# Performance work log

Hardware: AMD Instinct MI355X
Metric: run time of the kernel (lower is better)

The kernel has to match this reference:

```python
import jax, jax.numpy as jnp
import numpy as np


def leaky(x):
    return jnp.where(x > 0, x, 0.2 * x)


def conv(x, w, b, s, p):
    y = jax.lax.conv_general_dilated(x, w, (s, s), [(p, p), (p, p)],
                                     dimension_numbers=('NCHW', 'OIHW', 'NCHW'))
    return y + b[None, :, None, None]


def maxpool2s1(x):
    return jax.lax.reduce_window(x, -jnp.inf, jax.lax.max, (1, 1, 2, 2), (1, 1, 1, 1), 'VALID')


def bn_eval(x, g, b, m, v):
    scale = g / jnp.sqrt(v + 1e-5)
    return (x - m[None, :, None, None]) * scale[None, :, None, None] + b[None, :, None, None]


def adaptive_avg_pool(x, oh, ow):
    # matches torch AdaptiveAvgPool2d window rule: [floor(i*H/o), ceil((i+1)*H/o))
    B, C, H, W = x.shape
    rows = []
    for i in range(oh):
        hs, he = (i * H) // oh, -((-(i + 1) * H) // oh)
        cols = []
        for j in range(ow):
            ws, we = (j * W) // ow, -((-(j + 1) * W) // ow)
            cols.append(x[:, :, hs:he, ws:we].mean((2, 3)))
        rows.append(jnp.stack(cols, -1))
    return jnp.stack(rows, -2)  # [B,C,oh,ow]


def forward(x, tw1, tb1, tw2, tb2, tw3, tb3, tw4, tb4,
            sw1, sb1, bn1_g, bn1_b, bn1_m, bn1_v,
            sw2, sb2, bn2_g, bn2_b, bn2_m, bn2_v,
            cw, cb, ew1, eb1, ew2, eb2, ew3, eb3):
    B = x.shape[0]
    E, K = ew1.shape[0], 2
    # --- scout router (BN in eval mode with running stats) ---
    h = jax.nn.relu(bn_eval(conv(x, sw1, sb1, 4, 3), bn1_g, bn1_b, bn1_m, bn1_v))
    h = jax.nn.relu(bn_eval(conv(h, sw2, sb2, 2, 1), bn2_g, bn2_b, bn2_m, bn2_v))
    logits = h.mean((2, 3)) @ cw.T + cb                       # [B,E]
    gate = jax.nn.softmax(logits, axis=-1)
    topk_p, topk_i = jax.lax.top_k(gate, K)                   # [B,K]
    topk_p = topk_p / (topk_p.sum(-1, keepdims=True) + 1e-6)
    # --- shared trunk ---
    t = maxpool2s1(leaky(conv(x, tw1, tb1, 4, 1)))            # 224->56->55
    t = maxpool2s1(leaky(conv(t, tw2, tb2, 2, 2)))            # 55->28->27
    t = leaky(conv(t, tw3, tb3, 1, 1))                        # 27
    t = maxpool2s1(leaky(conv(t, tw4, tb4, 1, 1)))            # 27->26
    t = adaptive_avg_pool(t, 3, 3)                            # [B,128,3,3]
    flat = t.reshape(B, -1)                                   # [B,1152]
    # --- MoE head: dense per-expert MLP, masked weighted combine ---
    h1 = leaky(jnp.einsum('bi,eoi->beo', flat, ew1) + eb1[None])   # [B,E,1024]
    h2 = leaky(jnp.einsum('beh,eoh->beo', h1, ew2) + eb2[None])    # [B,E,512]
    h3 = jnp.einsum('beh,eoh->beo', h2, ew3) + eb3[None]           # [B,E,feat]
    onehot = (topk_i[:, :, None] == jnp.arange(E)[None, None, :])  # [B,K,E]
    comb_w = jnp.sum(topk_p[:, :, None] * onehot, axis=1)          # [B,E]
    out = jnp.einsum('beo,be->bo', h3, comb_w)                     # [B,feat]
    return out


def setup_inputs() -> dict:
    key = jax.random.key(0)
    ks = jax.random.split(key, 32)
    W = 0.02
    d = {}
    d['x'] = jax.random.normal(ks[0], (256, 3, 224, 224), jnp.float32)
    d['tw1'] = jax.random.normal(ks[1], (16, 3, 3, 3), jnp.float32) * W
    d['tb1'] = jnp.zeros((16,), jnp.float32)
    d['tw2'] = jax.random.normal(ks[2], (32, 16, 5, 5), jnp.float32) * W
    d['tb2'] = jnp.zeros((32,), jnp.float32)
    d['tw3'] = jax.random.normal(ks[3], (64, 32, 3, 3), jnp.float32) * W
    d['tb3'] = jnp.zeros((64,), jnp.float32)
    d['tw4'] = jax.random.normal(ks[4], (128, 64, 3, 3), jnp.float32) * W
    d['tb4'] = jnp.zeros((128,), jnp.float32)
    d['sw1'] = jax.random.normal(ks[5], (16, 3, 7, 7), jnp.float32) * W
    d['sb1'] = jnp.zeros((16,), jnp.float32)
    d['bn1_g'] = jnp.ones((16,), jnp.float32)
    d['bn1_b'] = jnp.zeros((16,), jnp.float32)
    d['bn1_m'] = jnp.zeros((16,), jnp.float32)
    d['bn1_v'] = jnp.ones((16,), jnp.float32)
    d['sw2'] = jax.random.normal(ks[6], (32, 16, 3, 3), jnp.float32) * W
    d['sb2'] = jnp.zeros((32,), jnp.float32)
    d['bn2_g'] = jnp.ones((32,), jnp.float32)
    d['bn2_b'] = jnp.zeros((32,), jnp.float32)
    d['bn2_m'] = jnp.zeros((32,), jnp.float32)
    d['bn2_v'] = jnp.ones((32,), jnp.float32)
    d['cw'] = jax.random.normal(ks[7], (3, 32), jnp.float32) * W
    d['cb'] = jnp.zeros((3,), jnp.float32)
    d['ew1'] = jax.random.normal(ks[8], (3, 1024, 1152), jnp.float32) * W
    d['eb1'] = jnp.zeros((3, 1024), jnp.float32)
    d['ew2'] = jax.random.normal(ks[9], (3, 512, 1024), jnp.float32) * W
    d['eb2'] = jnp.zeros((3, 512), jnp.float32)
    d['ew3'] = jax.random.normal(ks[10], (3, 512, 512), jnp.float32) * W
    d['eb3'] = jnp.zeros((3, 512), jnp.float32)
    return d


def reference(x, tw1, tb1, tw2, tb2, tw3, tb3, tw4, tb4,
              sw1, sb1, bn1_g, bn1_b, bn1_m, bn1_v,
              sw2, sb2, bn2_g, bn2_b, bn2_m, bn2_v,
              cw, cb, ew1, eb1, ew2, eb2, ew3, eb3):
    return forward(x, tw1, tb1, tw2, tb2, tw3, tb3, tw4, tb4,
                   sw1, sb1, bn1_g, bn1_b, bn1_m, bn1_v,
                   sw2, sb2, bn2_g, bn2_b, bn2_m, bn2_v,
                   cw, cb, ew1, eb1, ew2, eb2, ew3, eb3)
```

## Files before the change

kernel.cpp:

```cpp
#include <hip/hip_runtime.h>

#define DEV static __device__ __forceinline__

constexpr int BATCH = 256;

DEV float leakyf(float x){ return x > 0.f ? x : 0.2f * x; }

typedef _Float16 f16x8 __attribute__((ext_vector_type(8)));
typedef float f32x4 __attribute__((ext_vector_type(4)));

DEV f16x8 max8(f16x8 a, f16x8 b){
  f16x8 r;
  #pragma unroll
  for (int j = 0; j < 8; ++j) r[j] = a[j] > b[j] ? a[j] : b[j];
  return r;
}

template<int IC,int OC>
DEV void wpackM_body(int i, const float* __restrict__ w, _Float16* __restrict__ wp){
  constexpr int F = OC/16;
  int j = i & 7, L = (i >> 3) & 63, rest = i >> 9;
  int f = rest % F; int q2 = rest / F; int s = q2 % (IC/32); int t = q2 / (IC/32);
  int oc = f*16 + (L & 15), ic = s*32 + (L >> 4)*8 + j;
  wp[i] = (_Float16)w[((size_t)oc*IC + ic)*9 + t];
}

template<int OC,int K>
DEV void wpackS_body(int i, const float* __restrict__ w, _Float16* __restrict__ wp){
  constexpr int F = OC/16, KWP = (K+1)/2;
  int j = i & 7, L = (i >> 3) & 63, rest = i >> 9;
  int f = rest % F, s = rest / F;
  int kh = s / KWP, kwp = s % KWP;
  int k = (L >> 4)*8 + j;
  int kw = 2*kwp + (k >> 4), ic = k & 15;
  int oc = f*16 + (L & 15);
  float v = (kw < K) ? w[((size_t)(oc*16 + ic)*K + kh)*K + kw] : 0.f;
  wp[i] = (_Float16)v;
}

DEV void wpackF_body(int i, const float* __restrict__ sw1,
                     const float* __restrict__ tw1, _Float16* __restrict__ wp){
  int j = i & 7, L = (i >> 3) & 63, rest = i >> 9;
  int nf = rest & 1, s = rest >> 1;
  int k = s*32 + (L >> 4)*8 + j;
  int oc = L & 15;
  int t = k / 48, c = k % 48;
  int dr = (t >> 1) - 1, dc = (t & 1) - 1;
  int ic = c >> 4, pr = (c >> 2) & 3, pc = c & 3;
  float v = 0.f;
  if (nf == 0){
    int kh = 4*dr + pr + 3, kw = 4*dc + pc + 3;
    if (kh >= 0 && kh < 7 && kw >= 0 && kw < 7) v = sw1[((oc*3 + ic)*7 + kh)*7 + kw];
  } else {
    int kh = 4*dr + pr + 1, kw = 4*dc + pc + 1;
    if (kh >= 0 && kh < 3 && kw >= 0 && kw < 3) v = tw1[((oc*3 + ic)*3 + kh)*3 + kw];
  }
  wp[i] = (_Float16)v;
}

__global__ __launch_bounds__(256) void wpackAll_k(
    const float* __restrict__ tw3, _Float16* __restrict__ wpk3,
    const float* __restrict__ tw4, _Float16* __restrict__ wpk4,
    const float* __restrict__ tw2, _Float16* __restrict__ wp2,
    const float* __restrict__ sw2, _Float16* __restrict__ wps2,
    const float* __restrict__ sw1, const float* __restrict__ tw1,
    _Float16* __restrict__ wpf){
  const int b = blockIdx.x;
  if (b < 72){
    wpackM_body<32,64>(b*256 + threadIdx.x, tw3, wpk3);
  } else if (b < 360){
    wpackM_body<64,128>((b-72)*256 + threadIdx.x, tw4, wpk4);
  } else if (b < 420){
    wpackS_body<32,5>((b-360)*256 + threadIdx.x, tw2, wp2);
  } else if (b < 444){
    wpackS_body<32,3>((b-420)*256 + threadIdx.x, sw2, wps2);
  } else {
    wpackF_body((b-444)*256 + threadIdx.x, sw1, tw1, wpf);
  }
}

template<int KTOT>
__global__ __launch_bounds__(256) void wpackGh_k(const float* __restrict__ w, int N,
    _Float16* __restrict__ wp){
  const int NF = N >> 4, KT = KTOT >> 5;
  const int total = NF * KT * 512;
  const int e = blockIdx.y;
  w  += (size_t)e * N * KTOT;
  wp += (size_t)e * total;
  int i = blockIdx.x*256 + threadIdx.x;
  if (i >= total) return;
  int j = i & 7, L = (i >> 3) & 63, rest = i >> 9;
  int nf = rest % NF, t = rest / NF;
  int n = nf*16 + (L & 15), k = t*32 + (L >> 4)*8 + j;
  wp[i] = (_Float16)w[(size_t)n*KTOT + k];
}

__global__ __launch_bounds__(256) void fusedM_k(
    const float* __restrict__ x,
    const _Float16* __restrict__ W,
    const float* __restrict__ sb, const float* __restrict__ cb_,
    const float* __restrict__ g, const float* __restrict__ bt,
    const float* __restrict__ mn, const float* __restrict__ vr,
    _Float16* __restrict__ s1out, _Float16* __restrict__ c1out){
  __shared__ __align__(16) _Float16 Ah[3*58*64];
  const int tid = threadIdx.x;
  const int n = blockIdx.x / 28, oh0 = (blockIdx.x % 28) * 2;

  if (tid < 48){
    int rr = tid >> 4, side = (tid >> 3) & 1, q = tid & 7;
    int col = side ? 57 : 0;
    *(int4*)((char*)Ah + (((rr*58 + col) << 7) + q*16)) = (int4){0,0,0,0};
  }

  {
    const int m = tid & 63;
    const bool mok = (m < 56);
    const int cc = m + 1;
    int rc0 = tid >> 6;
    int ic   = (rc0 == 3) ? 0 : rc0;
    int ridx = (rc0 == 3) ? 1 : 0;
    #pragma unroll
    for (int j = 0; j < 9; ++j){
      const int ih = 4*oh0 - 4 + ridx;
      if (mok){
        float4 v = {0.f,0.f,0.f,0.f};
        if (ih >= 0)
          v = *(const float4*)(x + ((size_t)(n*3 + ic)*224 + ih)*224 + 4*m);
        const int rr = ridx >> 2, pr = ridx & 3;
        int boff = (((rr*58 + cc) << 7) + ic*32 + pr*8) ^ ((cc & 7) << 4);
        _Float16 h4[4] = {(_Float16)v.x, (_Float16)v.y, (_Float16)v.z, (_Float16)v.w};
        *(unsigned long long*)((char*)Ah + boff) = *(unsigned long long*)h4;
      }
      ic += 1; ridx += 1;
      if (ic >= 3){ ic -= 3; ridx += 1; }
    }
  }
  __syncthreads();

  const int wid = tid >> 6, lane = tid & 63;
  const int kg8 = (lane >> 4) * 8;
  f32x4 acc[2][2];
  #pragma unroll
  for (int mi = 0; mi < 2; ++mi)
    #pragma unroll
    for (int nf = 0; nf < 2; ++nf) acc[mi][nf] = (f32x4){0.f,0.f,0.f,0.f};

  #pragma unroll
  for (int s = 0; s < 6; ++s){
    const int kk = s*32 + kg8;
    const int t = kk / 48, c0 = kk - t*48;
    const int ra = t >> 1, ca = t & 1;
    f16x8 ah[2];
    #pragma unroll
    for (int mi = 0; mi < 2; ++mi){
      const int m = 2*wid + mi;
      const int rowsel = m >> 2;
      const int ow = (m & 3)*16 + (lane & 15);
      const int owc = ow > 55 ? 55 : ow;
      const int col = owc + ca;
      const int bidx = ((((rowsel + ra)*58 + col) << 7) + c0*2) ^ ((col & 7) << 4);
      ah[mi] = *(const f16x8*)((const char*)Ah + bidx);
    }
    #pragma unroll
    for (int nf = 0; nf < 2; ++nf){
      const f16x8 bw = *(const f16x8*)(W + (s*2 + nf)*512 + lane*8);
      #pragma unroll
      for (int mi = 0; mi < 2; ++mi)
        acc[mi][nf] = __builtin_amdgcn_mfma_f32_16x16x32_f16(ah[mi], bw, acc[mi][nf], 0,0,0);
    }
  }

  const int oc = lane & 15;
  const float sbv = sb[oc];
  const float scv = g[oc] * __frsqrt_rn(vr[oc] + 1e-5f);
  const float mnv = mn[oc], btv = bt[oc], cbv = cb_[oc];
  #pragma unroll
  for (int mi = 0; mi < 2; ++mi){
    const int m = 2*wid + mi;
    const int row = oh0 + (m >> 2);
    const int owb = (m & 3)*16 + (lane >> 4)*4;
    #pragma unroll
    for (int r = 0; r < 4; ++r){
      const int ow = owb + r;
      if (ow >= 56) continue;
      float vs = acc[mi][0][r] + sbv;
      vs = fmaxf((vs - mnv)*scv + btv, 0.f);
      const size_t o = (((size_t)n*56 + row)*56 + ow)*16 + oc;
      s1out[o] = (_Float16)vs;
      c1out[o] = (_Float16)leakyf(acc[mi][1][r] + cbv);
    }
  }
}

template<int OC,int K,int P,int IH,int IW,int ACT,bool OUT16,bool GATE,bool POOLIN>
__global__ __launch_bounds__(256) void convS_k(
    const _Float16* __restrict__ in,
    const _Float16* __restrict__ W,
    const float* __restrict__ bias,
    const float* __restrict__ bng, const float* __restrict__ bnb,
    const float* __restrict__ bnm, const float* __restrict__ bnv,
    float* __restrict__ outF, _Float16* __restrict__ outH,
    float* __restrict__ gsum){
  constexpr int F = OC/16, KWP = (K+1)/2;
  constexpr int RW = POOLIN ? (IW+1) : IW;
  __shared__ __align__(16) _Float16 A[K*60*16];
  __shared__ float gred[32];

  const int tid = threadIdx.x;
  const int n = blockIdx.x / 28, oh = blockIdx.x % 28;

  if (GATE && tid < 32) gred[tid] = 0.f;

  for (int i = tid; i < K*60*2; i += 256){
    int half = i & 1; int p = i >> 1;
    int c = p % 60; int r = p / 60;
    int ih = 2*oh - P + r, iw = c - P;
    int4 v = {0,0,0,0};
    if (ih >= 0 && ih < IH && iw >= 0 && iw < IW){
      const _Float16* q = in + (((size_t)n*(POOLIN ? IH+1 : IH) + ih)*RW + iw)*16 + half*8;
      if (POOLIN){
        f16x8 a = *(const f16x8*)q;
        f16x8 b = *(const f16x8*)(q + 16);
        f16x8 cc = *(const f16x8*)(q + RW*16);
        f16x8 d = *(const f16x8*)(q + RW*16 + 16);
        f16x8 mx = max8(max8(a, b), max8(cc, d));
        v = *(int4*)&mx;
      } else {
        v = *(const int4*)q;
      }
    }
    int byte = ((r*60 + c)*32 + half*16) ^ (((c>>1)&7) << 4);
    *(int4*)((char*)A + byte) = v;
  }
  __syncthreads();

  const int wid = tid >> 6, lane = tid & 63;
  const int fsel = wid & 1, mb = wid >> 1;
  const int ow_l = min(mb*16 + (lane & 15), 27);
  const int ic0b = ((lane >> 4) & 1) * 16;
  const int kwo  = (lane >> 4) >> 1;

  f32x4 acc = {0.f,0.f,0.f,0.f};
  #pragma unroll
  for (int kh = 0; kh < K; ++kh){
    #pragma unroll
    for (int kwp = 0; kwp < KWP; ++kwp){
      const int kw = 2*kwp + kwo;
      const int c = 2*ow_l + kw;
      int byte = ((kh*60 + c)*32 + ic0b) ^ (((c>>1)&7) << 4);
      f16x8 a = *(const f16x8*)((const char*)A + byte);
      const int s = kh*KWP + kwp;
      const f16x8 b = *(const f16x8*)(W + (s*F + fsel)*512 + lane*8);
      acc = __builtin_amdgcn_mfma_f32_16x16x32_f16(a, b, acc, 0,0,0);
    }
  }

  const int oc = fsel*16 + (lane & 15);
  float bv = bias[oc], sc = 1.f, mm = 0.f, bb = 0.f;
  if (ACT == 1){
    sc = bng[oc] * __frsqrt_rn(bnv[oc] + 1e-5f);
    mm = bnm[oc]; bb = bnb[oc];
  }
  float lsum = 0.f;
  #pragma unroll
  for (int r = 0; r < 4; ++r){
    const int ow = mb*16 + (lane >> 4)*4 + r;
    if (ow >= 28) continue;
    float v = acc[r] + bv;
    if (ACT == 1) v = fmaxf((v - mm)*sc + bb, 0.f);
    else          v = leakyf(v);
    if (GATE){
      lsum += v;
    } else {
      const size_t o = (((size_t)n*28 + oh)*28 + ow)*OC + oc;
      if (OUT16) outH[o] = (_Float16)v;
      else       outF[o] = v;
    }
  }
  if (GATE){
    atomicAdd(&gred[oc], lsum);
    __syncthreads();
    if (tid < 32) atomicAdd(&gsum[n*32 + tid], gred[tid]);
  }
}

template<int IC,int OC,bool POOLIN>
__global__ __launch_bounds__(256) void convM_k(
    const _Float16* __restrict__ Ag,
    const _Float16* __restrict__ W,
    const float* __restrict__ bias,
    _Float16* __restrict__ Out)
{
  constexpr int S = IC/32, FTOT = OC/16, FW = FTOT/2;
  constexpr int ICB = IC*2, ICG = ICB/16;
  __shared__ __align__(16) char A[4*34*ICB];

  const int tid = threadIdx.x;
  const int bx = blockIdx.x;
  const int n = bx / 14, pr = bx % 14;
  const int oh0 = pr * 2;

  for (int g = tid; g < 4*34*ICG; g += 256){
    int r = g / (34*ICG);
    int rem = g - r*(34*ICG);
    int c = rem / ICG, q = rem - c*ICG;
    int ir = oh0 + r - 1, icol = c - 1;
    int4 v = {0,0,0,0};
    if (ir >= 0 && ir < 27 && icol >= 0 && icol < 27){
      if (POOLIN){
        const _Float16* p0 = Ag + (((size_t)n*28 + ir)*28 + icol)*IC + q*8;
        f16x8 a = *(const f16x8*)p0;
        f16x8 b = *(const f16x8*)(p0 + IC);
        f16x8 cc = *(const f16x8*)(p0 + 28*IC);
        f16x8 d = *(const f16x8*)(p0 + 28*IC + IC);
        f16x8 mx = max8(max8(a, b), max8(cc, d));
        v = *(int4*)&mx;
      } else {
        v = *(const int4*)(Ag + (((size_t)n*27 + ir)*27 + icol)*IC + q*8);
      }
    }
    int off = (r*34 + c)*ICB + q*16;
    int swz = off ^ ((c & 7) << 4);
    *(int4*)(A + swz) = v;
  }
  __syncthreads();

  const int wid = tid >> 6, lane = tid & 63;
  const int rsel = wid & 1, ocq = wid >> 1;
  const int c0 = lane & 15, kg = (lane >> 4) * 16;
  const int colb0 = c0*ICB + kg, colb1 = (16 + c0)*ICB + kg;
  int msk[3];
  #pragma unroll
  for (int kw = 0; kw < 3; ++kw) msk[kw] = ((c0 + kw) & 7) << 4;

  f32x4 acc[2][FW];
  #pragma unroll
  for (int m = 0; m < 2; ++m)
    #pragma unroll
    for (int f = 0; f < FW; ++f) acc[m][f] = (f32x4){0.f,0.f,0.f,0.f};

  #pragma unroll
  for (int kh = 0; kh < 3; ++kh){
    #pragma unroll
    for (int kw = 0; kw < 3; ++kw){
      #pragma unroll
      for (int s = 0; s < S; ++s){
        const int fr0 = (((kh*3 + kw)*S + s)*FTOT + ocq*FW) * 512 + lane*8;
        f16x8 b[FW];
        #pragma unroll
        for (int f = 0; f < FW; ++f)
          b[f] = *(const f16x8*)(W + fr0 + f*512);
        const int base = ((rsel + kh)*34 + kw)*ICB + s*64;
        const int o0 = (base + colb0) ^ msk[kw];
        const int o1 = (base + colb1) ^ msk[kw];
        f16x8 a0 = *(const f16x8*)(A + o0);
        f16x8 a1 = *(const f16x8*)(A + o1);
        #pragma unroll
        for (int f = 0; f < FW; ++f){
          acc[0][f] = __builtin_amdgcn_mfma_f32_16x16x32_f16(a0, b[f], acc[0][f], 0,0,0);
          acc[1][f] = __builtin_amdgcn_mfma_f32_16x16x32_f16(a1, b[f], acc[1][f], 0,0,0);
        }
      }
    }
  }

  const int orow = oh0 + rsel;
  if (orow >= 27) return;
  #pragma unroll
  for (int f = 0; f < FW; ++f){
    const int oc = (ocq*FW + f)*16 + c0;
    const float bv = bias[oc];
    #pragma unroll
    for (int m = 0; m < 2; ++m){
      #pragma unroll
      for (int r = 0; r < 4; ++r){
        const int ow = m*16 + (lane >> 4)*4 + r;
        if (ow >= 27) continue;
        float v = leakyf(acc[m][f][r] + bv);
        Out[(((size_t)n*27 + orow)*27 + ow)*OC + oc] = (_Float16)v;
      }
    }
  }
}

template<int KTOT,int ACT>
__global__ __launch_bounds__(256) void gemmH_k(
    const _Float16* __restrict__ A, long strideA,
    const _Float16* __restrict__ W,
    const float* __restrict__ bias, int N,
    _Float16* __restrict__ OutH){
  const int e = blockIdx.z;
  A += (size_t)e * strideA;
  const int NF = N >> 4, KT = KTOT >> 5;
  W += (size_t)e * NF * KT * 512;
  const float* bs = bias + (size_t)e * N;
  const size_t ob = (size_t)e * 256 * N;

  const int tid = threadIdx.x, wid = tid >> 6, lane = tid & 63;
  const int mblk = blockIdx.x * 32;
  const int nf = blockIdx.y * 4 + wid;
  const int r0 = mblk + (lane & 15);
  const int kof = (lane >> 4) * 8;

  f32x4 acc0 = {0,0,0,0}, acc1 = {0,0,0,0};
  for (int t = 0; t < KT; ++t){
    const int k = t*32 + kof;
    f16x8 a0 = *(const f16x8*)(A + (size_t)r0*KTOT + k);
    f16x8 a1 = *(const f16x8*)(A + (size_t)(r0+16)*KTOT + k);
    const f16x8 b = *(const f16x8*)(W + ((size_t)t*NF + nf)*512 + lane*8);
    acc0 = __builtin_amdgcn_mfma_f32_16x16x32_f16(a0, b, acc0, 0,0,0);
    acc1 = __builtin_amdgcn_mfma_f32_16x16x32_f16(a1, b, acc1, 0,0,0);
  }
  const int n = nf*16 + (lane & 15);
  const float bv = bs[n];
  #pragma unroll
  for (int mi = 0; mi < 2; ++mi){
    f32x4 a = mi ? acc1 : acc0;
    #pragma unroll
    for (int r = 0; r < 4; ++r){
      const int m = mblk + mi*16 + (lane >> 4)*4 + r;
      float v = a[r] + bv;
      if (ACT == 1) v = leakyf(v);
      OutH[ob + (size_t)m*N + n] = (_Float16)v;
    }
  }
}

__global__ __launch_bounds__(256) void gemmC_k(
    const _Float16* __restrict__ A,
    const _Float16* __restrict__ W,
    const float* __restrict__ b3,
    const float* __restrict__ combw,
    float* __restrict__ out){
  const int tid = threadIdx.x, wid = tid >> 6, lane = tid & 63;
  const int mblk = blockIdx.x * 16;
  const int nf = blockIdx.y * 4 + wid;
  const int r0 = mblk + (lane & 15);
  const int kof = (lane >> 4) * 8;
  const int n = nf*16 + (lane & 15);

  f32x4 oacc = {0.f,0.f,0.f,0.f};
  #pragma unroll
  for (int e = 0; e < 3; ++e){
    const _Float16* Ae = A + (size_t)e * 256 * 512;
    const _Float16* We = W + (size_t)e * 32 * 16 * 512;
    f32x4 acc = {0.f,0.f,0.f,0.f};
    for (int t = 0; t < 16; ++t){
      f16x8 a = *(const f16x8*)(Ae + (size_t)r0*512 + t*32 + kof);
      const f16x8 b = *(const f16x8*)(We + ((size_t)t*32 + nf)*512 + lane*8);
      acc = __builtin_amdgcn_mfma_f32_16x16x32_f16(a, b, acc, 0,0,0);
    }
    const float bv = b3[e*512 + n];
    #pragma unroll
    for (int r = 0; r < 4; ++r){
      const int m = mblk + (lane >> 4)*4 + r;
      oacc[r] += combw[m*3 + e] * (acc[r] + bv);
    }
  }
  #pragma unroll
  for (int r = 0; r < 4; ++r){
    const int m = mblk + (lane >> 4)*4 + r;
    out[(size_t)m*512 + n] = oacc[r];
  }
}

__global__ __launch_bounds__(256) void gate2_k(const float* __restrict__ gsum,
                                               const float* __restrict__ cw,
                                               const float* __restrict__ cb,
                                               float* __restrict__ comb){
  int n = blockIdx.x * 256 + threadIdx.x;
  if (n >= BATCH) return;
  float mch[32];
  #pragma unroll
  for (int c = 0; c < 32; ++c) mch[c] = gsum[n*32 + c] / 784.f;
  float lg[3];
  #pragma unroll
  for (int e = 0; e < 3; ++e){
    float a = cb[e];
    #pragma unroll
    for (int c = 0; c < 32; ++c) a += mch[c] * cw[e*32 + c];
    lg[e] = a;
  }
  float m = fmaxf(lg[0], fmaxf(lg[1], lg[2]));
  float ex[3], sum = 0.f;
  #pragma unroll
  for (int e = 0; e < 3; ++e){ ex[e] = expf(lg[e] - m); sum += ex[e]; }
  float pr[3];
  #pragma unroll
  for (int e = 0; e < 3; ++e) pr[e] = ex[e] / sum;
  int i1 = 0;
  if (pr[1] > pr[0]) i1 = 1;
  if (pr[2] > pr[i1]) i1 = 2;
  int i2 = -1;
  for (int e = 0; e < 3; ++e){
    if (e == i1) continue;
    if (i2 < 0 || pr[e] > pr[i2]) i2 = e;
  }
  float s12 = pr[i1] + pr[i2] + 1e-6f;
  float cmb[3] = {0.f, 0.f, 0.f};
  cmb[i1] = pr[i1] / s12;
  cmb[i2] = pr[i2] / s12;
  comb[n*3 + 0] = cmb[0];
  comb[n*3 + 1] = cmb[1];
  comb[n*3 + 2] = cmb[2];
}

__global__ __launch_bounds__(256) void papool2_k(const _Float16* __restrict__ in,
                                                 _Float16* __restrict__ flat16){
  __shared__ float red[2][128][9];
  const int n = blockIdx.x;
  const int tid = threadIdx.x;
  const int h = tid >> 7, c = tid & 127;
  const _Float16* p = in + (size_t)n * 729 * 128 + c;

  float sum[9];
  #pragma unroll
  for (int j = 0; j < 9; ++j) sum[j] = 0.f;

  float prev[27], cur[27];
  const int r0 = h * 13;
  #pragma unroll
  for (int rr = 0; rr < 14; ++rr){
    const int r = r0 + rr;
    #pragma unroll
    for (int cc = 0; cc < 27; ++cc)
      cur[cc] = (float)p[(size_t)(r*27 + cc) * 128];
    if (rr > 0){
      const int pr = r - 1;
      const bool b0 = (pr < 9), b1 = (pr >= 8) && (pr < 18), b2 = (pr >= 17);
      #pragma unroll
      for (int cc = 0; cc < 26; ++cc){
        float v = fmaxf(fmaxf(prev[cc], prev[cc+1]), fmaxf(cur[cc], cur[cc+1]));
        if (b0){
          if (cc < 9)             sum[0] += v;
          if (cc >= 8 && cc < 18) sum[1] += v;
          if (cc >= 17)           sum[2] += v;
        }
        if (b1){
          if (cc < 9)             sum[3] += v;
          if (cc >= 8 && cc < 18) sum[4] += v;
          if (cc >= 17)           sum[5] += v;
        }
        if (b2){
          if (cc < 9)             sum[6] += v;
          if (cc >= 8 && cc < 18) sum[7] += v;
          if (cc >= 17)           sum[8] += v;
        }
      }
    }
    #pragma unroll
    for (int cc = 0; cc < 27; ++cc) prev[cc] = cur[cc];
  }

  #pragma unroll
  for (int j = 0; j < 9; ++j) red[h][c][j] = sum[j];
  __syncthreads();

  if (tid < 128){
    const float rcp[9] = {1.f/81, 1.f/90, 1.f/81, 1.f/90, 1.f/100, 1.f/90,
                          1.f/81, 1.f/90, 1.f/81};
    _Float16* o = flat16 + (size_t)n * 1152 + tid * 9;
    #pragma unroll
    for (int j = 0; j < 9; ++j)
      o[j] = (_Float16)((red[0][tid][j] + red[1][tid][j]) * rcp[j]);
  }
}

extern "C" void kernel_launch(void* const* d_in, const int* in_sizes, int n_in,
                              void* d_out, int out_size, void* d_ws, size_t ws_size,
                              hipStream_t stream){
  const float* x    = (const float*)d_in[0];
  const float* tw1  = (const float*)d_in[1];  const float* tb1 = (const float*)d_in[2];
  const float* tw2  = (const float*)d_in[3];  const float* tb2 = (const float*)d_in[4];
  const float* tw3  = (const float*)d_in[5];  const float* tb3 = (const float*)d_in[6];
  const float* tw4  = (const float*)d_in[7];  const float* tb4 = (const float*)d_in[8];
  const float* sw1  = (const float*)d_in[9];  const float* sb1 = (const float*)d_in[10];
  const float* bn1g = (const float*)d_in[11]; const float* bn1b = (const float*)d_in[12];
  const float* bn1m = (const float*)d_in[13]; const float* bn1v = (const float*)d_in[14];
  const float* sw2  = (const float*)d_in[15]; const float* sb2 = (const float*)d_in[16];
  const float* bn2g = (const float*)d_in[17]; const float* bn2b = (const float*)d_in[18];
  const float* bn2m = (const float*)d_in[19]; const float* bn2v = (const float*)d_in[20];
  const float* cw   = (const float*)d_in[21]; const float* cb  = (const float*)d_in[22];
  const float* ew1  = (const float*)d_in[23]; const float* eb1 = (const float*)d_in[24];
  const float* ew2  = (const float*)d_in[25]; const float* eb2 = (const float*)d_in[26];
  const float* ew3  = (const float*)d_in[27]; const float* eb3 = (const float*)d_in[28];
  float* out = (float*)d_out;

  float* ws = (float*)d_ws;
  size_t off = 0;
  float* comb   = ws + off; off += 768;
  _Float16* flat16 = (_Float16*)(ws + off); off += 147456;
  float* gsum   = ws + off; off += BATCH * 32;
  _Float16* wpk3 = (_Float16*)(ws + off); off += 9216;
  _Float16* wpk4 = (_Float16*)(ws + off); off += 36864;
  _Float16* wp2  = (_Float16*)(ws + off); off += 7680;
  _Float16* wps2 = (_Float16*)(ws + off); off += 3072;
  _Float16* wpf  = (_Float16*)(ws + off); off += 3072;
  off += 16;
  float* bufA   = ws + off; off += 13778944;
  off += 16;
  float* bufB   = ws + off; off += 23887872;
  off += 16;
  (void)ws_size; (void)in_sizes; (void)n_in; (void)out_size;

  _Float16* s1h = (_Float16*)bufA;
  _Float16* c1h = (_Float16*)bufB;
  _Float16* c2h = (_Float16*)(bufB + 14000000);
  _Float16* C3u = (_Float16*)bufA;
  _Float16* c4h = (_Float16*)bufB;

  _Float16* hb = (_Float16*)bufB;
  size_t uo = 0;
  _Float16* ewp1 = hb + uo; uo += 3538944;
  _Float16* ewp2 = hb + uo; uo += 1572864;
  _Float16* ewp3 = hb + uo; uo += 786432;
  _Float16* h1   = hb + uo; uo += 786432;
  _Float16* h2   = hb + uo; uo += 393216;

  dim3 blk(256);

  hipMemsetAsync(gsum, 0, BATCH * 32 * sizeof(float), stream);
  wpackAll_k<<<dim3(468), blk, 0, stream>>>(
      tw3, wpk3, tw4, wpk4, tw2, wp2, sw2, wps2, sw1, tw1, wpf);

  fusedM_k<<<dim3(BATCH*28), blk, 0, stream>>>(
      x, wpf, sb1, tb1, bn1g, bn1b, bn1m, bn1v, s1h, c1h);

  convS_k<32,3,1,56,56,1,false,true,false><<<dim3(BATCH*28), blk, 0, stream>>>(
      s1h, wps2, sb2, bn2g, bn2b, bn2m, bn2v, nullptr, nullptr, gsum);
  gate2_k<<<dim3(1), blk, 0, stream>>>(gsum, cw, cb, comb);

  convS_k<32,5,2,55,55,0,true,false,true><<<dim3(BATCH*28), blk, 0, stream>>>(
      c1h, wp2, tb2, nullptr, nullptr, nullptr, nullptr, nullptr, c2h, nullptr);

  convM_k<32,64,true><<<dim3(BATCH*14), blk, 0, stream>>>(
      c2h, wpk3, tb3, C3u);

  convM_k<64,128,false><<<dim3(BATCH*14), blk, 0, stream>>>(
      C3u, wpk4, tb4, c4h);

  papool2_k<<<dim3(BATCH), blk, 0, stream>>>(c4h, flat16);

  wpackGh_k<1152><<<dim3(4608,3), blk, 0, stream>>>(ew1, 1024, ewp1);
  wpackGh_k<1024><<<dim3(2048,3), blk, 0, stream>>>(ew2,  512, ewp2);
  wpackGh_k< 512><<<dim3(1024,3), blk, 0, stream>>>(ew3,  512, ewp3);

  gemmH_k<1152,1><<<dim3(8,16,3), blk, 0, stream>>>(
      flat16, 0L, ewp1, eb1, 1024, h1);
  gemmH_k<1024,1><<<dim3(8,8,3), blk, 0, stream>>>(
      h1, 256L*1024, ewp2, eb2, 512, h2);
  gemmC_k<<<dim3(16,8), blk, 0, stream>>>(
      h2, ewp3, eb3, comb, out);
}
```

Baseline: 265.9 us.

## Merge kernel launches: fold expert weight packing, both small convs, and gating

Folds the three expert-weight packing kernels into the initial weight-pack kernel, merges the two independent small convolutions into one launch split by block index, and moves the gate softmax/top-k computation into the final combine GEMM. Buffers are reassigned so the packed expert weights live in bufA beyond the activations that use it. The aim is fewer kernel launches and serialization gaps, and letting independent work share the GPU. The merged conv kernel uses the larger shared-memory footprint for both halves, which may reduce occupancy, and gate logic is recomputed per block of the final GEMM.

Result: faster. 257.1 us (-3.3%).

```diff
diff --git a/kernel.cpp b/kernel.cpp
--- a/kernel.cpp
+++ b/kernel.cpp
@@ -58,41 +58,53 @@
   wp[i] = (_Float16)v;
 }
 
-__global__ __launch_bounds__(256) void wpackAll_k(
+template<int KTOT>
+DEV void wpackG_body(int i, int e, const float* __restrict__ w, int N,
+                     _Float16* __restrict__ wp){
+  const int NF = N >> 4;
+  const int total = NF * (KTOT >> 5) * 512;
+  w  += (size_t)e * N * KTOT;
+  wp += (size_t)e * total;
+  int j = i & 7, L = (i >> 3) & 63, rest = i >> 9;
+  int nf = rest % NF, t = rest / NF;
+  int n = nf*16 + (L & 15), k = t*32 + (L >> 4)*8 + j;
+  wp[i] = (_Float16)w[(size_t)n*KTOT + k];
+}
+
+__global__ __launch_bounds__(256) void wpackX_k(
     const float* __restrict__ tw3, _Float16* __restrict__ wpk3,
     const float* __restrict__ tw4, _Float16* __restrict__ wpk4,
     const float* __restrict__ tw2, _Float16* __restrict__ wp2,
     const float* __restrict__ sw2, _Float16* __restrict__ wps2,
     const float* __restrict__ sw1, const float* __restrict__ tw1,
-    _Float16* __restrict__ wpf){
+    _Float16* __restrict__ wpf,
+    const float* __restrict__ ew1, _Float16* __restrict__ ewp1,
+    const float* __restrict__ ew2, _Float16* __restrict__ ewp2,
+    const float* __restrict__ ew3, _Float16* __restrict__ ewp3){
   const int b = blockIdx.x;
+  const int tid = threadIdx.x;
   if (b < 72){
-    wpackM_body<32,64>(b*256 + threadIdx.x, tw3, wpk3);
+    wpackM_body<32,64>(b*256 + tid, tw3, wpk3);
   } else if (b < 360){
-    wpackM_body<64,128>((b-72)*256 + threadIdx.x, tw4, wpk4);
+    wpackM_body<64,128>((b-72)*256 + tid, tw4, wpk4);
   } else if (b < 420){
-    wpackS_body<32,5>((b-360)*256 + threadIdx.x, tw2, wp2);
+    wpackS_body<32,5>((b-360)*256 + tid, tw2, wp2);
   } else if (b < 444){
-    wpackS_body<32,3>((b-420)*256 + threadIdx.x, sw2, wps2);
+    wpackS_body<32,3>((b-420)*256 + tid, sw2, wps2);
+  } else if (b < 468){
+    wpackF_body((b-444)*256 + tid, sw1, tw1, wpf);
   } else {
-    wpackF_body((b-444)*256 + threadIdx.x, sw1, tw1, wpf);
-  }
-}
-
-template<int KTOT>
-__global__ __launch_bounds__(256) void wpackGh_k(const float* __restrict__ w, int N,
-    _Float16* __restrict__ wp){
-  const int NF = N >> 4, KT = KTOT >> 5;
-  const int total = NF * KT * 512;
-  const int e = blockIdx.y;
-  w  += (size_t)e * N * KTOT;
-  wp += (size_t)e * total;
-  int i = blockIdx.x*256 + threadIdx.x;
-  if (i >= total) return;
-  int j = i & 7, L = (i >> 3) & 63, rest = i >> 9;
-  int nf = rest % NF, t = rest / NF;
-  int n = nf*16 + (L & 15), k = t*32 + (L >> 4)*8 + j;
-  wp[i] = (_Float16)w[(size_t)n*KTOT + k];
+    int t = b - 468;
+    if (t < 13824){
+      wpackG_body<1152>((t % 4608)*256 + tid, t / 4608, ew1, 1024, ewp1);
+    } else if (t < 19968){
+      int t2 = t - 13824;
+      wpackG_body<1024>((t2 % 2048)*256 + tid, t2 / 2048, ew2, 512, ewp2);
+    } else {
+      int t3 = t - 19968;
+      wpackG_body<512>((t3 % 1024)*256 + tid, t3 / 1024, ew3, 512, ewp3);
+    }
+  }
 }
 
 __global__ __launch_bounds__(256) void fusedM_k(
@@ -193,7 +205,7 @@
 }
 
 template<int OC,int K,int P,int IH,int IW,int ACT,bool OUT16,bool GATE,bool POOLIN>
-__global__ __launch_bounds__(256) void convS_k(
+DEV void convS_body(int bx, int tid, _Float16* A, float* gred,
     const _Float16* __restrict__ in,
     const _Float16* __restrict__ W,
     const float* __restrict__ bias,
@@ -203,11 +215,8 @@
     float* __restrict__ gsum){
   constexpr int F = OC/16, KWP = (K+1)/2;
   constexpr int RW = POOLIN ? (IW+1) : IW;
-  __shared__ __align__(16) _Float16 A[K*60*16];
-  __shared__ float gred[32];
-
-  const int tid = threadIdx.x;
-  const int n = blockIdx.x / 28, oh = blockIdx.x % 28;
+
+  const int n = bx / 28, oh = bx % 28;
 
   if (GATE && tid < 32) gred[tid] = 0.f;
 
@@ -281,6 +290,26 @@
     atomicAdd(&gred[oc], lsum);
     __syncthreads();
     if (tid < 32) atomicAdd(&gsum[n*32 + tid], gred[tid]);
+  }
+}
+
+__global__ __launch_bounds__(256) void convSS_k(
+    const _Float16* __restrict__ s1h, const _Float16* __restrict__ wps2,
+    const float* __restrict__ sb2,
+    const float* __restrict__ bn2g, const float* __restrict__ bn2b,
+    const float* __restrict__ bn2m, const float* __restrict__ bn2v,
+    float* __restrict__ gsum,
+    const _Float16* __restrict__ c1h, const _Float16* __restrict__ wp2,
+    const float* __restrict__ tb2, _Float16* __restrict__ c2h){
+  __shared__ __align__(16) _Float16 A[5*60*16];
+  __shared__ float gred[32];
+  const int tid = threadIdx.x;
+  if (blockIdx.x < BATCH*28){
+    convS_body<32,3,1,56,56,1,false,true,false>(blockIdx.x, tid, A, gred,
+        s1h, wps2, sb2, bn2g, bn2b, bn2m, bn2v, nullptr, nullptr, gsum);
+  } else {
+    convS_body<32,5,2,55,55,0,true,false,true>(blockIdx.x - BATCH*28, tid, A, gred,
+        c1h, wp2, tb2, nullptr, nullptr, nullptr, nullptr, nullptr, c2h, nullptr);
   }
 }
 
@@ -430,10 +459,51 @@
     const _Float16* __restrict__ A,
     const _Float16* __restrict__ W,
     const float* __restrict__ b3,
-    const float* __restrict__ combw,
+    const float* __restrict__ gsum,
+    const float* __restrict__ cw, const float* __restrict__ cb,
     float* __restrict__ out){
+  __shared__ float combL[16][3];
   const int tid = threadIdx.x, wid = tid >> 6, lane = tid & 63;
   const int mblk = blockIdx.x * 16;
+
+  if (tid < 16){
+    const int n = mblk + tid;
+    float mch[32];
+    #pragma unroll
+    for (int c = 0; c < 32; ++c) mch[c] = gsum[n*32 + c] / 784.f;
+    float lg[3];
+    #pragma unroll
+    for (int e = 0; e < 3; ++e){
+      float a = cb[e];
+      #pragma unroll
+      for (int c = 0; c < 32; ++c) a += mch[c] * cw[e*32 + c];
+      lg[e] = a;
+    }
+    float m = fmaxf(lg[0], fmaxf(lg[1], lg[2]));
+    float ex[3], sum = 0.f;
+    #pragma unroll
+    for (int e = 0; e < 3; ++e){ ex[e] = expf(lg[e] - m); sum += ex[e]; }
+    float pr[3];
+    #pragma unroll
+    for (int e = 0; e < 3; ++e) pr[e] = ex[e] / sum;
+    int i1 = 0;
+    if (pr[1] > pr[0]) i1 = 1;
+    if (pr[2] > pr[i1]) i1 = 2;
+    int i2 = -1;
+    for (int e = 0; e < 3; ++e){
+      if (e == i1) continue;
+      if (i2 < 0 || pr[e] > pr[i2]) i2 = e;
+    }
+    float s12 = pr[i1] + pr[i2] + 1e-6f;
+    float cmb[3] = {0.f, 0.f, 0.f};
+    cmb[i1] = pr[i1] / s12;
+    cmb[i2] = pr[i2] / s12;
+    combL[tid][0] = cmb[0];
+    combL[tid][1] = cmb[1];
+    combL[tid][2] = cmb[2];
+  }
+  __syncthreads();
+
   const int nf = blockIdx.y * 4 + wid;
   const int r0 = mblk + (lane & 15);
   const int kof = (lane >> 4) * 8;
@@ -453,8 +523,8 @@
     const float bv = b3[e*512 + n];
     #pragma unroll
     for (int r = 0; r < 4; ++r){
-      const int m = mblk + (lane >> 4)*4 + r;
-      oacc[r] += combw[m*3 + e] * (acc[r] + bv);
+      const int lr = (lane >> 4)*4 + r;
+      oacc[r] += combL[lr][e] * (acc[r] + bv);
     }
   }
   #pragma unroll
@@ -462,47 +532,6 @@
     const int m = mblk + (lane >> 4)*4 + r;
     out[(size_t)m*512 + n] = oacc[r];
   }
-}
-
-__global__ __launch_bounds__(256) void gate2_k(const float* __restrict__ gsum,
-                                               const float* __restrict__ cw,
-                                               const float* __restrict__ cb,
-                                               float* __restrict__ comb){
-  int n = blockIdx.x * 256 + threadIdx.x;
-  if (n >= BATCH) return;
-  float mch[32];
-  #pragma unroll
-  for (int c = 0; c < 32; ++c) mch[c] = gsum[n*32 + c] / 784.f;
-  float lg[3];
-  #pragma unroll
-  for (int e = 0; e < 3; ++e){
-    float a = cb[e];
-    #pragma unroll
-    for (int c = 0; c < 32; ++c) a += mch[c] * cw[e*32 + c];
-    lg[e] = a;
-  }
-  float m = fmaxf(lg[0], fmaxf(lg[1], lg[2]));
-  float ex[3], sum = 0.f;
-  #pragma unroll
-  for (int e = 0; e < 3; ++e){ ex[e] = expf(lg[e] - m); sum += ex[e]; }
-  float pr[3];
-  #pragma unroll
-  for (int e = 0; e < 3; ++e) pr[e] = ex[e] / sum;
-  int i1 = 0;
-  if (pr[1] > pr[0]) i1 = 1;
-  if (pr[2] > pr[i1]) i1 = 2;
-  int i2 = -1;
-  for (int e = 0; e < 3; ++e){
-    if (e == i1) continue;
-    if (i2 < 0 || pr[e] > pr[i2]) i2 = e;
-  }
-  float s12 = pr[i1] + pr[i2] + 1e-6f;
-  float cmb[3] = {0.f, 0.f, 0.f};
-  cmb[i1] = pr[i1] / s12;
-  cmb[i2] = pr[i2] / s12;
-  comb[n*3 + 0] = cmb[0];
-  comb[n*3 + 1] = cmb[1];
-  comb[n*3 + 2] = cmb[2];
 }
 
 __global__ __launch_bounds__(256) void papool2_k(const _Float16* __restrict__ in,
@@ -588,7 +617,6 @@
 
   float* ws = (float*)d_ws;
   size_t off = 0;
-  float* comb   = ws + off; off += 768;
   _Float16* flat16 = (_Float16*)(ws + off); off += 147456;
   float* gsum   = ws + off; off += BATCH * 32;
   _Float16* wpk3 = (_Float16*)(ws + off); off += 9216;
@@ -604,34 +632,29 @@
   (void)ws_size; (void)in_sizes; (void)n_in; (void)out_size;
 
   _Float16* s1h = (_Float16*)bufA;
+  _Float16* C3u = (_Float16*)bufA;
+  _Float16* ewp1 = (_Float16*)(bufA + 6500000);
+  _Float16* ewp2 = ewp1 + 3538944;
+  _Float16* ewp3 = ewp2 + 1572864;
   _Float16* c1h = (_Float16*)bufB;
   _Float16* c2h = (_Float16*)(bufB + 14000000);
-  _Float16* C3u = (_Float16*)bufA;
   _Float16* c4h = (_Float16*)bufB;
-
-  _Float16* hb = (_Float16*)bufB;
-  size_t uo = 0;
-  _Float16* ewp1 = hb + uo; uo += 3538944;
-  _Float16* ewp2 = hb + uo; uo += 1572864;
-  _Float16* ewp3 = hb + uo; uo += 786432;
-  _Float16* h1   = hb + uo; uo += 786432;
-  _Float16* h2   = hb + uo; uo += 393216;
+  _Float16* h1  = (_Float16*)bufB;
+  _Float16* h2  = h1 + 786432;
 
   dim3 blk(256);
 
   hipMemsetAsync(gsum, 0, BATCH * 32 * sizeof(float), stream);
-  wpackAll_k<<<dim3(468), blk, 0, stream>>>(
-      tw3, wpk3, tw4, wpk4, tw2, wp2, sw2, wps2, sw1, tw1, wpf);
+  wpackX_k<<<dim3(23508), blk, 0, stream>>>(
+      tw3, wpk3, tw4, wpk4, tw2, wp2, sw2, wps2, sw1, tw1, wpf,
+      ew1, ewp1, ew2, ewp2, ew3, ewp3);
 
   fusedM_k<<<dim3(BATCH*28), blk, 0, stream>>>(
       x, wpf, sb1, tb1, bn1g, bn1b, bn1m, bn1v, s1h, c1h);
 
-  convS_k<32,3,1,56,56,1,false,true,false><<<dim3(BATCH*28), blk, 0, stream>>>(
-      s1h, wps2, sb2, bn2g, bn2b, bn2m, bn2v, nullptr, nullptr, gsum);
-  gate2_k<<<dim3(1), blk, 0, stream>>>(gsum, cw, cb, comb);
-
-  convS_k<32,5,2,55,55,0,true,false,true><<<dim3(BATCH*28), blk, 0, stream>>>(
-      c1h, wp2, tb2, nullptr, nullptr, nullptr, nullptr, nullptr, c2h, nullptr);
+  convSS_k<<<dim3(BATCH*28*2), blk, 0, stream>>>(
+      s1h, wps2, sb2, bn2g, bn2b, bn2m, bn2v, gsum,
+      c1h, wp2, tb2, c2h);
 
   convM_k<32,64,true><<<dim3(BATCH*14), blk, 0, stream>>>(
       c2h, wpk3, tb3, C3u);
@@ -640,15 +663,11 @@
       C3u, wpk4, tb4, c4h);
 
   papool2_k<<<dim3(BATCH), blk, 0, stream>>>(c4h, flat16);
-
-  wpackGh_k<1152><<<dim3(4608,3), blk, 0, stream>>>(ew1, 1024, ewp1);
-  wpackGh_k<1024><<<dim3(2048,3), blk, 0, stream>>>(ew2,  512, ewp2);
-  wpackGh_k< 512><<<dim3(1024,3), blk, 0, stream>>>(ew3,  512, ewp3);
 
   gemmH_k<1152,1><<<dim3(8,16,3), blk, 0, stream>>>(
       flat16, 0L, ewp1, eb1, 1024, h1);
   gemmH_k<1024,1><<<dim3(8,8,3), blk, 0, stream>>>(
       h1, 256L*1024, ewp2, eb2, 512, h2);
   gemmC_k<<<dim3(16,8), blk, 0, stream>>>(
-      h2, ewp3, eb3, comb, out);
-}
+      h2, ewp3, eb3, gsum, cw, cb, out);
+}
```
